# Performance work log

Hardware: AMD Instinct MI355X
Metric: run time of the kernel (lower is better)

The kernel has to match this reference:

```python
import jax, jax.numpy as jnp
import numpy as np

N_ING, N_DIR = 100000, 50000
E = 1000000
H, D = 4, 16          # heads, per-head dim
HID = H * D           # 64
LAT, COND = 32, 8
F_ING, F_DIR = 16, 8
OUT_ING = 16


def _han_edge(x_src, x_dst, att_s, att_d, edge_index, n_dst):
    # HANConv per-edge-type attention message passing.
    src, dst = edge_index[0], edge_index[1]
    a = jax.nn.leaky_relu(
        jnp.einsum('nhd,hd->nh', x_src, att_s)[src]
        + jnp.einsum('nhd,hd->nh', x_dst, att_d)[dst],
        negative_slope=0.2)                               # [E, H]
    amax = jax.ops.segment_max(a, dst, num_segments=n_dst)
    ex = jnp.exp(a - amax[dst])
    denom = jax.ops.segment_sum(ex, dst, num_segments=n_dst)
    alpha = ex / (denom[dst] + 1e-16)                     # PyG softmax eps
    out = jax.ops.segment_sum(x_src[src] * alpha[:, :, None], dst,
                              num_segments=n_dst)         # [n_dst, H, D]
    return jax.nn.relu(out.reshape(n_dst, HID))


def _group(outs, q, Wk, bk):
    # HANConv semantic-level attention across edge types.
    s = jnp.stack(outs)                                   # [T, N, HID]
    score = jnp.tanh(s @ Wk + bk).mean(axis=1) @ q        # [T]
    attn = jax.nn.softmax(score)
    return jnp.einsum('t,tnf->nf', attn, s)


def setup_inputs() -> dict:
    key = jax.random.key(0)
    ks = jax.random.split(key, 32)
    def ei(k, n_src, n_dst):
        k1, k2 = jax.random.split(k)
        return jnp.stack([jax.random.randint(k1, (E,), 0, n_src),
                          jax.random.randint(k2, (E,), 0, n_dst)]).astype(jnp.int64)
    s = 0.1
    inp = {
        'x_ing': jax.random.normal(ks[0], (N_ING, F_ING), jnp.float32),
        'x_dir': jax.random.normal(ks[1], (N_DIR, F_DIR), jnp.float32),
        'cond':  jax.random.normal(ks[2], (COND,), jnp.float32),
        'eps':   jax.random.normal(ks[3], (1, LAT), jnp.float32),
        'ei_cooc':     ei(ks[4], N_ING, N_DIR),
        'ei_used':     ei(ks[5], N_ING, N_DIR),
        'ei_contains': ei(ks[6], N_DIR, N_ING),
        'ei_pairs':    ei(ks[7], N_DIR, N_DIR),
        'ei_follows':  ei(ks[8], N_DIR, N_DIR),
        # node-type projections
        'W_pi': jax.random.normal(ks[9],  (F_ING, HID)) * s,
        'b_pi': jnp.zeros((HID,)),
        'W_pd': jax.random.normal(ks[10], (F_DIR, HID)) * s,
        'b_pd': jnp.zeros((HID,)),
        # semantic attention
        'Wk': jax.random.normal(ks[21], (HID, HID)) * s,
        'bk': jnp.zeros((HID,)),
        'q':  jax.random.normal(ks[22], (HID,)) * s,
        # VAE heads (input: 2*HID + COND)
        'W_mu': jax.random.normal(ks[23], (2 * HID + COND, LAT)) * s,
        'b_mu': jnp.zeros((LAT,)),
        'W_lv': jax.random.normal(ks[24], (2 * HID + COND, LAT)) * s,
        'b_lv': jnp.zeros((LAT,)),
        # decoder (fc1 is dead code in the original forward)
        'W_fc3': jax.random.normal(ks[25], (LAT, HID)) * s,
        'b_fc3': jnp.zeros((HID,)),
        'W_fc2': jax.random.normal(ks[26], (HID, OUT_ING)) * s,
        'b_fc2': jnp.zeros((OUT_ING,)),
    }
    for i, name in enumerate(['cooc', 'used', 'contains', 'pairs', 'follows']):
        inp[f'as_{name}'] = jax.random.normal(ks[11 + i], (H, D)) * s
        inp[f'ad_{name}'] = jax.random.normal(ks[16 + i], (H, D)) * s
    return inp


def reference(x_ing, x_dir, cond, eps,
              ei_cooc, ei_used, ei_contains, ei_pairs, ei_follows,
              W_pi, b_pi, W_pd, b_pd,
              as_cooc, ad_cooc, as_used, ad_used, as_contains, ad_contains,
              as_pairs, ad_pairs, as_follows, ad_follows,
              Wk, bk, q, W_mu, b_mu, W_lv, b_lv,
              W_fc3, b_fc3, W_fc2, b_fc2):
    # node-type projections -> [N, H, D]
    h_ing = (x_ing @ W_pi + b_pi).reshape(N_ING, H, D)
    h_dir = (x_dir @ W_pd + b_pd).reshape(N_DIR, H, D)

    o_cooc = _han_edge(h_ing, h_dir, as_cooc, ad_cooc, ei_cooc, N_DIR)
    o_used = _han_edge(h_ing, h_dir, as_used, ad_used, ei_used, N_DIR)
    o_cont = _han_edge(h_dir, h_ing, as_contains, ad_contains, ei_contains, N_ING)
    o_pair = _han_edge(h_dir, h_dir, as_pairs, ad_pairs, ei_pairs, N_DIR)
    o_foll = _han_edge(h_dir, h_dir, as_follows, ad_follows, ei_follows, N_DIR)

    out_ing = _group([o_cont], q, Wk, bk)                       # [N_ING, HID]
    out_dir = _group([o_cooc, o_used, o_pair, o_foll], q, Wk, bk)

    ingre_pool = out_ing.mean(axis=0, keepdims=True)            # [1, HID]
    direc_pool = out_dir.mean(axis=0, keepdims=True)
    graph_repr = jnp.concatenate([ingre_pool, direc_pool, cond[None]], axis=1)

    mu = graph_repr @ W_mu + b_mu
    logvar = graph_repr @ W_lv + b_lv
    z = mu + eps * jnp.exp(0.5 * logvar)

    # decoder: fc1 branch is overwritten in the original; effective path below
    recon = jnp.tanh(jax.nn.relu(z @ W_fc3 + b_fc3) @ W_fc2 + b_fc2)  # [1, OUT_ING]
    return recon, mu, logvar
```

## Files before the change

kernel.cpp:

```cpp
#include <hip/hip_runtime.h>
#include <hip/hip_fp16.h>
#include <math.h>

#define N_ING 100000
#define N_DIR 50000
#define NE    1000000
#define NDST_TOTAL 300000
#define NBUCK 4688
#define BA    16
#define NBK   (5 * BA)
#define I4PT  (NE / 4)
#define PB_ING 384
#define PB_DIR 192

typedef float v2f __attribute__((ext_vector_type(2)));

__global__ __launch_bounds__(256) void kA_kernel(
    const int* __restrict__ e0, const int* __restrict__ e1,
    const int* __restrict__ e2, const int* __restrict__ e3,
    const int* __restrict__ e4, int* __restrict__ blockcnt,
    const float* __restrict__ x_ing, const float* __restrict__ W_pi,
    const float* __restrict__ b_pi,
    const float* __restrict__ as_cooc, const float* __restrict__ as_used,
    const float* __restrict__ ad_contains,
    unsigned* __restrict__ h8_ing, __half* __restrict__ s_ing,
    const float* __restrict__ x_dir, const float* __restrict__ W_pd,
    const float* __restrict__ b_pd,
    const float* __restrict__ ad_cooc, const float* __restrict__ ad_used,
    const float* __restrict__ as_contains, const float* __restrict__ as_pairs,
    const float* __restrict__ ad_pairs, const float* __restrict__ as_follows,
    const float* __restrict__ ad_follows,
    unsigned* __restrict__ h8_dir, __half* __restrict__ s_dir)
{
    __shared__ int hist[NBUCK];
    __shared__ float sW[16 * 64];
    __shared__ float sbb[64];
    __shared__ float satt[7 * 64];
    __shared__ float sx[4][16];
    __shared__ float srow[4][64];

    const int bid = blockIdx.x;
    const int tid = threadIdx.x;
    if (bid < NBK) {
        const int type = bid / BA, blk = bid % BA;
        const int* ei = type == 0 ? e0 : type == 1 ? e1 : type == 2 ? e2
                      : type == 3 ? e3 : e4;
        const int base = type == 0 ? 0 : type == 1 ? 50000 : type == 2 ? 100000
                       : type == 3 ? 200000 : 250000;
        for (int i = tid; i < NBUCK; i += 256) hist[i] = 0;
        __syncthreads();
        const int4* d4 = (const int4*)(ei + NE);
        for (int i = blk * 256 + tid; i < I4PT; i += BA * 256) {
            int4 d = d4[i];
            atomicAdd(&hist[(base + d.x) >> 6], 1);
            atomicAdd(&hist[(base + d.y) >> 6], 1);
            atomicAdd(&hist[(base + d.z) >> 6], 1);
            atomicAdd(&hist[(base + d.w) >> 6], 1);
        }
        __syncthreads();
        int* row = blockcnt + (size_t)bid * NBUCK;
        for (int i = tid; i < NBUCK; i += 256) row[i] = hist[i];
    } else if (bid < NBK + PB_ING) {
        const int g = tid >> 6, t = tid & 63;
        for (int i = tid; i < 16 * 64; i += 256) sW[i] = W_pi[i];
        if (tid < 64) {
            sbb[tid] = b_pi[tid];
            satt[tid]       = as_cooc[tid];
            satt[64 + tid]  = as_used[tid];
            satt[128 + tid] = ad_contains[tid];
        }
        __syncthreads();
        for (int q = bid - NBK; q < N_ING / 4; q += PB_ING) {
            int n = q * 4 + g;
            if (t < 16) sx[g][t] = x_ing[(size_t)n * 16 + t];
            __syncthreads();
            float s = sbb[t];
#pragma unroll
            for (int i = 0; i < 16; ++i) s += sx[g][i] * sW[i * 64 + t];
            srow[g][t] = s;
            __syncthreads();
            if (t < 16) {
                int w0 = __builtin_amdgcn_cvt_pk_fp8_f32(srow[g][t * 4], srow[g][t * 4 + 1], 0, false);
                int w  = __builtin_amdgcn_cvt_pk_fp8_f32(srow[g][t * 4 + 2], srow[g][t * 4 + 3], w0, true);
                h8_ing[(size_t)n * 16 + t] = (unsigned)w;
            }
            if (t < 12) {
                int slot = t >> 2, hh = t & 3;
                float sc = 0.f;
#pragma unroll
                for (int d = 0; d < 16; ++d)
                    sc += srow[g][hh * 16 + d] * satt[slot * 64 + hh * 16 + d];
                s_ing[(size_t)n * 12 + t] = __float2half(sc);
            }
            __syncthreads();
        }
    } else {
        const int g = tid >> 6, t = tid & 63;
        for (int i = tid; i < 8 * 64; i += 256) sW[i] = W_pd[i];
        if (tid < 64) {
            sbb[tid] = b_pd[tid];
            satt[tid]        = ad_cooc[tid];
            satt[64  + tid]  = ad_used[tid];
            satt[128 + tid]  = as_contains[tid];
            satt[192 + tid]  = as_pairs[tid];
            satt[256 + tid]  = ad_pairs[tid];
            satt[320 + tid]  = as_follows[tid];
            satt[384 + tid]  = ad_follows[tid];
        }
        __syncthreads();
        for (int q = bid - NBK - PB_ING; q < N_DIR / 4; q += PB_DIR) {
            int n = q * 4 + g;
            if (t < 8) sx[g][t] = x_dir[(size_t)n * 8 + t];
            __syncthreads();
            float s = sbb[t];
#pragma unroll
            for (int i = 0; i < 8; ++i) s += sx[g][i] * sW[i * 64 + t];
            srow[g][t] = s;
            __syncthreads();
            if (t < 16) {
                int w0 = __builtin_amdgcn_cvt_pk_fp8_f32(srow[g][t * 4], srow[g][t * 4 + 1], 0, false);
                int w  = __builtin_amdgcn_cvt_pk_fp8_f32(srow[g][t * 4 + 2], srow[g][t * 4 + 3], w0, true);
                h8_dir[(size_t)n * 16 + t] = (unsigned)w;
            }
            if (t < 28) {
                int slot = t >> 2, hh = t & 3;
                float sc = 0.f;
#pragma unroll
                for (int d = 0; d < 16; ++d)
                    sc += srow[g][hh * 16 + d] * satt[slot * 64 + hh * 16 + d];
                s_dir[(size_t)n * 28 + t] = __float2half(sc);
            }
            __syncthreads();
        }
    }
}

__global__ __launch_bounds__(256) void k2_kernel(
    const int* __restrict__ blockcnt, int* __restrict__ blockbase,
    int* __restrict__ bbase, int* __restrict__ btot, int* __restrict__ cursor)
{
    __shared__ int part[4][64];
    __shared__ int tots[64];
    __shared__ int scn[64];
    __shared__ int bw;
    const int tid = threadIdx.x;
    const int kq = tid >> 6, bl = tid & 63;
    const int b = blockIdx.x * 64 + bl;
    const int K = NBK / 4;
    int ps = 0;
    if (b < NBUCK)
        for (int k = kq * K; k < kq * K + K; ++k)
            ps += blockcnt[(size_t)k * NBUCK + b];
    part[kq][bl] = ps;
    __syncthreads();
    if (tid < 64) {
        int t = part[0][tid] + part[1][tid] + part[2][tid] + part[3][tid];
        tots[tid] = t;
        scn[tid] = t;
    }
    __syncthreads();
    for (int off = 1; off < 64; off <<= 1) {
        int v = 0;
        if (tid < 64 && tid >= off) v = scn[tid - off];
        __syncthreads();
        if (tid < 64) scn[tid] += v;
        __syncthreads();
    }
    if (tid == 63) bw = atomicAdd(cursor, scn[63]);
    __syncthreads();
    if (b < NBUCK) {
        int bs = bw + scn[bl] - tots[bl];
        if (kq == 0) {
            bbase[b] = bs;
            btot[b] = tots[bl];
        }
        int run = bs;
        for (int q = 0; q < kq; ++q) run += part[q][bl];
        for (int k = kq * K; k < kq * K + K; ++k) {
            blockbase[(size_t)k * NBUCK + b] = run;
            run += blockcnt[(size_t)k * NBUCK + b];
        }
    }
}

__global__ __launch_bounds__(256) void k3_kernel(
    const int* __restrict__ e0, const int* __restrict__ e1,
    const int* __restrict__ e2, const int* __restrict__ e3,
    const int* __restrict__ e4, const int* __restrict__ blockbase,
    unsigned* __restrict__ bpair)
{
    __shared__ int cur[NBUCK];
    const int bid = blockIdx.x, tid = threadIdx.x;
    const int type = bid / BA, blk = bid % BA;
    const int* ei = type == 0 ? e0 : type == 1 ? e1 : type == 2 ? e2
                  : type == 3 ? e3 : e4;
    const int base = type == 0 ? 0 : type == 1 ? 50000 : type == 2 ? 100000
                   : type == 3 ? 200000 : 250000;
    const int* row = blockbase + (size_t)bid * NBUCK;
    for (int i = tid; i < NBUCK; i += 256) cur[i] = row[i];
    __syncthreads();
    const int4* s4 = (const int4*)ei;
    const int4* d4 = (const int4*)(ei + NE);
    for (int i = blk * 256 + tid; i < I4PT; i += BA * 256) {
        int4 s = s4[i];
        int4 d = d4[i];
        int g0 = base + d.x, g1 = base + d.y, g2 = base + d.z, g3 = base + d.w;
        int p0 = atomicAdd(&cur[g0 >> 6], 1);
        int p1 = atomicAdd(&cur[g1 >> 6], 1);
        int p2 = atomicAdd(&cur[g2 >> 6], 1);
        int p3 = atomicAdd(&cur[g3 >> 6], 1);
        bpair[p0] = ((unsigned)(g0 & 63) << 17) | (unsigned)s.x;
        bpair[p1] = ((unsigned)(g1 & 63) << 17) | (unsigned)s.y;
        bpair[p2] = ((unsigned)(g2 & 63) << 17) | (unsigned)s.z;
        bpair[p3] = ((unsigned)(g3 & 63) << 17) | (unsigned)s.w;
    }
}

__global__ __launch_bounds__(256) void k4_kernel(
    const unsigned* __restrict__ bpair, const int* __restrict__ bbase,
    const int* __restrict__ btot, int* __restrict__ perm,
    int* __restrict__ start, int* __restrict__ cnt)
{
    __shared__ int h[64], sc[64], cu[64];
    const int b = blockIdx.x, tid = threadIdx.x;
    const int jb = bbase[b], n = btot[b];
    if (tid < 64) h[tid] = 0;
    __syncthreads();
    for (int i = tid; i < n; i += 256)
        atomicAdd(&h[bpair[jb + i] >> 17], 1);
    __syncthreads();
    if (tid == 0) {
        int r = 0;
        for (int i = 0; i < 64; ++i) { sc[i] = r; cu[i] = r; r += h[i]; }
    }
    __syncthreads();
    if (tid < 64) {
        int dg = b * 64 + tid;
        if (dg < NDST_TOTAL) {
            start[dg] = jb + sc[tid];
            cnt[dg] = h[tid];
        }
    }
    for (int i = tid; i < n; i += 256) {
        unsigned p = bpair[jb + i];
        int pos = atomicAdd(&cu[p >> 17], 1);
        perm[jb + pos] = (int)(p & 0x1FFFF);
    }
}

__global__ __launch_bounds__(256) void agg_all_kernel(
    const int* __restrict__ perm, const int* __restrict__ start,
    const int* __restrict__ cnttot,
    const unsigned* __restrict__ h8_ing, const unsigned* __restrict__ h8_dir,
    const __half* __restrict__ s_ing, const __half* __restrict__ s_dir,
    const float* __restrict__ Wk, const float* __restrict__ bk,
    float* __restrict__ pool_ing, float* __restrict__ pool_dir,
    float* __restrict__ sem_dir)
{
    __shared__ float sWk[64 * 64];
    __shared__ float srow[4][64];
    __shared__ float sred[4][64];
    const int t = threadIdx.x & 63, w = threadIdx.x >> 6;
    const int g  = t >> 4;
    const int l4 = t & 15;
    const int hq = l4 >> 2;
    for (int i = threadIdx.x; i < 4096; i += 256) sWk[i] = Wk[i];
    const float bkf = bk[t];
    float p_ing = 0.f;
    float p0 = 0.f, p1 = 0.f, p2 = 0.f, p3 = 0.f;
    float m0 = 0.f, m1 = 0.f, m2 = 0.f, m3 = 0.f;
    __syncthreads();
    const int nwaves = gridDim.x * 4;
    for (int d = blockIdx.x * 4 + w; d < NDST_TOTAL; d += nwaves) {
        int type, ld;
        const __half *ssrc, *sdst;
        const unsigned* hsrc;
        int ss, soff, ds, doff;
        if (d < 50000)       { type = 0; ld = d;          ssrc = s_ing; ss = 12; soff = 0;  sdst = s_dir; ds = 28; doff = 0;  hsrc = h8_ing; }
        else if (d < 100000) { type = 1; ld = d - 50000;  ssrc = s_ing; ss = 12; soff = 4;  sdst = s_dir; ds = 28; doff = 4;  hsrc = h8_ing; }
        else if (d < 200000) { type = 2; ld = d - 100000; ssrc = s_dir; ss = 28; soff = 8;  sdst = s_ing; ds = 12; doff = 8;  hsrc = h8_dir; }
        else if (d < 250000) { type = 3; ld = d - 200000; ssrc = s_dir; ss = 28; soff = 12; sdst = s_dir; ds = 28; doff = 16; hsrc = h8_dir; }
        else                 { type = 4; ld = d - 250000; ssrc = s_dir; ss = 28; soff = 20; sdst = s_dir; ds = 28; doff = 24; hsrc = h8_dir; }
        float adst = __half2float(sdst[(size_t)ld * ds + doff + hq]);
        int jb = start[d], je = jb + cnttot[d];
        float4 acc = make_float4(0.f, 0.f, 0.f, 0.f);
        float dsum = 0.f;
        for (int j = jb; j < je; j += 8) {
            int j0 = j + g, j1 = j + 4 + g;
            bool v0 = j0 < je, v1 = j1 < je;
            int s0 = perm[v0 ? j0 : je - 1];
            int s1 = perm[v1 ? j1 : je - 1];
            float c0 = __half2float(ssrc[(size_t)s0 * ss + soff + hq]);
            float c1 = __half2float(ssrc[(size_t)s1 * ss + soff + hq]);
            unsigned u0 = hsrc[(size_t)s0 * 16 + l4];
            unsigned u1 = hsrc[(size_t)s1 * 16 + l4];
            float a0 = c0 + adst; a0 = a0 > 0.f ? a0 : 0.2f * a0;
            float a1 = c1 + adst; a1 = a1 > 0.f ? a1 : 0.2f * a1;
            float e0 = v0 ? __expf(a0) : 0.f;
            float e1 = v1 ? __expf(a1) : 0.f;
            dsum += e0 + e1;
            v2f lo0 = __builtin_amdgcn_cvt_pk_f32_fp8((int)u0, false);
            v2f hi0 = __builtin_amdgcn_cvt_pk_f32_fp8((int)u0, true);
            v2f lo1 = __builtin_amdgcn_cvt_pk_f32_fp8((int)u1, false);
            v2f hi1 = __builtin_amdgcn_cvt_pk_f32_fp8((int)u1, true);
            acc.x += lo0.x * e0 + lo1.x * e1;
            acc.y += lo0.y * e0 + lo1.y * e1;
            acc.z += hi0.x * e0 + hi1.x * e1;
            acc.w += hi0.y * e0 + hi1.y * e1;
        }
#pragma unroll
        for (int mask = 16; mask <= 32; mask <<= 1) {
            acc.x += __shfl_xor(acc.x, mask, 64);
            acc.y += __shfl_xor(acc.y, mask, 64);
            acc.z += __shfl_xor(acc.z, mask, 64);
            acc.w += __shfl_xor(acc.w, mask, 64);
            dsum  += __shfl_xor(dsum,  mask, 64);
        }
        float inv = 1.f / (dsum + 1e-16f);
        float4 v4 = make_float4(fmaxf(acc.x * inv, 0.f), fmaxf(acc.y * inv, 0.f),
                                fmaxf(acc.z * inv, 0.f), fmaxf(acc.w * inv, 0.f));
        if (g == 0) *(float4*)&srow[w][l4 * 4] = v4;
        float v = srow[w][t];
        if (type == 2) {
            p_ing += v;
        } else {
            float a2 = bkf;
#pragma unroll
            for (int k = 0; k < 64; ++k) a2 += srow[w][k] * sWk[k * 64 + t];
            float tv = tanhf(a2);
            if (type == 0)      { p0 += v; m0 += tv; }
            else if (type == 1) { p1 += v; m1 += tv; }
            else if (type == 3) { p2 += v; m2 += tv; }
            else                { p3 += v; m3 += tv; }
        }
    }
    float vals[9] = { p_ing, p0, p1, p2, p3, m0, m1, m2, m3 };
    float* outs[9] = { pool_ing, pool_dir, pool_dir + 64, pool_dir + 128,
                       pool_dir + 192, sem_dir, sem_dir + 64, sem_dir + 128,
                       sem_dir + 192 };
    for (int i = 0; i < 9; ++i) {
        __syncthreads();
        sred[w][t] = vals[i];
        __syncthreads();
        if (w == 0)
            atomicAdd(&outs[i][t], sred[0][t] + sred[1][t] + sred[2][t] + sred[3][t]);
    }
}

__global__ __launch_bounds__(64) void final_kernel(
    const float* __restrict__ pool_ing, const float* __restrict__ pool_dir,
    const float* __restrict__ sem_dir, const float* __restrict__ q,
    const float* __restrict__ cond, const float* __restrict__ eps,
    const float* __restrict__ W_mu, const float* __restrict__ b_mu,
    const float* __restrict__ W_lv, const float* __restrict__ b_lv,
    const float* __restrict__ W_fc3, const float* __restrict__ b_fc3,
    const float* __restrict__ W_fc2, const float* __restrict__ b_fc2,
    float* __restrict__ out)
{
    __shared__ float gr[136];
    __shared__ float sc[4], attn[4];
    __shared__ float z[32], hfc[64];
    int t = threadIdx.x;
    if (t < 4) {
        float s = 0.f;
        for (int f = 0; f < 64; ++f)
            s += (sem_dir[t * 64 + f] / (float)N_DIR) * q[f];
        sc[t] = s;
    }
    gr[t] = pool_ing[t] / (float)N_ING;
    __syncthreads();
    if (t == 0) {
        float m = fmaxf(fmaxf(sc[0], sc[1]), fmaxf(sc[2], sc[3]));
        float ssum = 0.f;
        for (int i = 0; i < 4; ++i) { attn[i] = expf(sc[i] - m); ssum += attn[i]; }
        for (int i = 0; i < 4; ++i) attn[i] /= ssum;
    }
    __syncthreads();
    {
        float v = 0.f;
        for (int tt = 0; tt < 4; ++tt)
            v += attn[tt] * (pool_dir[tt * 64 + t] / (float)N_DIR);
        gr[64 + t] = v;
    }
    if (t < 8) gr[128 + t] = cond[t];
    __syncthreads();
    if (t < 32) {
        float m = b_mu[t], lv = b_lv[t];
        for (int i = 0; i < 136; ++i) {
            float g = gr[i];
            m  += g * W_mu[i * 32 + t];
            lv += g * W_lv[i * 32 + t];
        }
        out[16 + t] = m;
        out[48 + t] = lv;
        z[t] = m + eps[t] * expf(0.5f * lv);
    }
    __syncthreads();
    {
        float v = b_fc3[t];
        for (int j = 0; j < 32; ++j) v += z[j] * W_fc3[j * 64 + t];
        hfc[t] = fmaxf(v, 0.f);
    }
    __syncthreads();
    if (t < 16) {
        float v = b_fc2[t];
        for (int f = 0; f < 64; ++f) v += hfc[f] * W_fc2[f * 16 + t];
        out[t] = tanhf(v);
    }
}

extern "C" void kernel_launch(void* const* d_in, const int* in_sizes, int n_in,
                              void* d_out, int out_size, void* d_ws, size_t ws_size,
                              hipStream_t stream) {
    const float* x_ing = (const float*)d_in[0];
    const float* x_dir = (const float*)d_in[1];
    const float* cond  = (const float*)d_in[2];
    const float* eps   = (const float*)d_in[3];
    const int* ei_cooc     = (const int*)d_in[4];
    const int* ei_used     = (const int*)d_in[5];
    const int* ei_contains = (const int*)d_in[6];
    const int* ei_pairs    = (const int*)d_in[7];
    const int* ei_follows  = (const int*)d_in[8];
    const float* W_pi = (const float*)d_in[9];
    const float* b_pi = (const float*)d_in[10];
    const float* W_pd = (const float*)d_in[11];
    const float* b_pd = (const float*)d_in[12];
    const float* Wk   = (const float*)d_in[13];
    const float* bk   = (const float*)d_in[14];
    const float* q    = (const float*)d_in[15];
    const float* W_mu = (const float*)d_in[16];
    const float* b_mu = (const float*)d_in[17];
    const float* W_lv = (const float*)d_in[18];
    const float* b_lv = (const float*)d_in[19];
    const float* W_fc3 = (const float*)d_in[20];
    const float* b_fc3 = (const float*)d_in[21];
    const float* W_fc2 = (const float*)d_in[22];
    const float* b_fc2 = (const float*)d_in[23];
    const float* as_cooc     = (const float*)d_in[24];
    const float* ad_cooc     = (const float*)d_in[25];
    const float* as_used     = (const float*)d_in[26];
    const float* ad_used     = (const float*)d_in[27];
    const float* as_contains = (const float*)d_in[28];
    const float* ad_contains = (const float*)d_in[29];
    const float* as_pairs    = (const float*)d_in[30];
    const float* ad_pairs    = (const float*)d_in[31];
    const float* as_follows  = (const float*)d_in[32];
    const float* ad_follows  = (const float*)d_in[33];

    unsigned* bpair = (unsigned*)d_ws;
    unsigned* h8_ing = bpair + (size_t)5 * NE;
    unsigned* h8_dir = h8_ing + (size_t)N_ING * 16;
    __half* s_ing = (__half*)(h8_dir + (size_t)N_DIR * 16);
    __half* s_dir = s_ing + (size_t)N_ING * 12;
    int*   perm  = (int*)(s_dir + (size_t)N_DIR * 28);
    int*   blockcnt  = perm + (size_t)5 * NE;
    int*   blockbase = blockcnt + (size_t)NBK * NBUCK;
    int*   bbase  = blockbase + (size_t)NBK * NBUCK;
    int*   btot   = bbase + NBUCK;
    int*   start  = btot + NBUCK;
    int*   cnt    = start + NDST_TOTAL;
    int*   cursor = cnt + NDST_TOTAL;
    float* pool_ing = (float*)(cursor + 1);
    float* pool_dir = pool_ing + 64;
    float* sem_dir  = pool_dir + 256;

    hipMemsetAsync(cursor, 0, (1 + 64 + 256 + 256) * sizeof(int), stream);

    kA_kernel<<<NBK + PB_ING + PB_DIR, 256, 0, stream>>>(
        ei_cooc, ei_used, ei_contains, ei_pairs, ei_follows, blockcnt,
        x_ing, W_pi, b_pi, as_cooc, as_used, ad_contains, h8_ing, s_ing,
        x_dir, W_pd, b_pd, ad_cooc, ad_used, as_contains, as_pairs, ad_pairs,
        as_follows, ad_follows, h8_dir, s_dir);

    k2_kernel<<<(NBUCK + 63) / 64, 256, 0, stream>>>(
        blockcnt, blockbase, bbase, btot, cursor);

    k3_kernel<<<NBK, 256, 0, stream>>>(
        ei_cooc, ei_used, ei_contains, ei_pairs, ei_follows, blockbase, bpair);

    k4_kernel<<<NBUCK, 256, 0, stream>>>(bpair, bbase, btot, perm, start, cnt);

    agg_all_kernel<<<2048, 256, 0, stream>>>(
        perm, start, cnt, h8_ing, h8_dir, s_ing, s_dir, Wk, bk,
        pool_ing, pool_dir, sem_dir);

    final_kernel<<<1, 64, 0, stream>>>(
        pool_ing, pool_dir, sem_dir, q, cond, eps,
        W_mu, b_mu, W_lv, b_lv, W_fc3, b_fc3, W_fc2, b_fc2, (float*)d_out);
}
```

Baseline: 541.2 us.

## Keep Wk column in registers, use exp2 with prescaled scores, 32-bit indexing

```diff
diff --git a/kernel.cpp b/kernel.cpp
--- a/kernel.cpp
+++ b/kernel.cpp
@@ -12,6 +12,7 @@
 #define I4PT  (NE / 4)
 #define PB_ING 384
 #define PB_DIR 192
+#define LOG2E 1.442695041f
 
 typedef float v2f __attribute__((ext_vector_type(2)));
 
@@ -65,9 +66,9 @@
         for (int i = tid; i < 16 * 64; i += 256) sW[i] = W_pi[i];
         if (tid < 64) {
             sbb[tid] = b_pi[tid];
-            satt[tid]       = as_cooc[tid];
-            satt[64 + tid]  = as_used[tid];
-            satt[128 + tid] = ad_contains[tid];
+            satt[tid]       = as_cooc[tid] * LOG2E;
+            satt[64 + tid]  = as_used[tid] * LOG2E;
+            satt[128 + tid] = ad_contains[tid] * LOG2E;
         }
         __syncthreads();
         for (int q = bid - NBK; q < N_ING / 4; q += PB_ING) {
@@ -99,13 +100,13 @@
         for (int i = tid; i < 8 * 64; i += 256) sW[i] = W_pd[i];
         if (tid < 64) {
             sbb[tid] = b_pd[tid];
-            satt[tid]        = ad_cooc[tid];
-            satt[64  + tid]  = ad_used[tid];
-            satt[128 + tid]  = as_contains[tid];
-            satt[192 + tid]  = as_pairs[tid];
-            satt[256 + tid]  = ad_pairs[tid];
-            satt[320 + tid]  = as_follows[tid];
-            satt[384 + tid]  = ad_follows[tid];
+            satt[tid]        = ad_cooc[tid] * LOG2E;
+            satt[64  + tid]  = ad_used[tid] * LOG2E;
+            satt[128 + tid]  = as_contains[tid] * LOG2E;
+            satt[192 + tid]  = as_pairs[tid] * LOG2E;
+            satt[256 + tid]  = ad_pairs[tid] * LOG2E;
+            satt[320 + tid]  = as_follows[tid] * LOG2E;
+            satt[384 + tid]  = ad_follows[tid] * LOG2E;
         }
         __syncthreads();
         for (int q = bid - NBK - PB_ING; q < N_DIR / 4; q += PB_DIR) {
@@ -248,7 +249,7 @@
     }
 }
 
-__global__ __launch_bounds__(256) void agg_all_kernel(
+__global__ __launch_bounds__(256, 4) void agg_all_kernel(
     const int* __restrict__ perm, const int* __restrict__ start,
     const int* __restrict__ cnttot,
     const unsigned* __restrict__ h8_ing, const unsigned* __restrict__ h8_dir,
@@ -257,47 +258,50 @@
     float* __restrict__ pool_ing, float* __restrict__ pool_dir,
     float* __restrict__ sem_dir)
 {
-    __shared__ float sWk[64 * 64];
-    __shared__ float srow[4][64];
+    __shared__ __align__(16) float srow[4][64];
     __shared__ float sred[4][64];
     const int t = threadIdx.x & 63, w = threadIdx.x >> 6;
     const int g  = t >> 4;
     const int l4 = t & 15;
     const int hq = l4 >> 2;
-    for (int i = threadIdx.x; i < 4096; i += 256) sWk[i] = Wk[i];
+
+    float wkc[64];
+#pragma unroll
+    for (int k = 0; k < 64; ++k) wkc[k] = Wk[k * 64 + t];
     const float bkf = bk[t];
+
     float p_ing = 0.f;
     float p0 = 0.f, p1 = 0.f, p2 = 0.f, p3 = 0.f;
     float m0 = 0.f, m1 = 0.f, m2 = 0.f, m3 = 0.f;
-    __syncthreads();
     const int nwaves = gridDim.x * 4;
     for (int d = blockIdx.x * 4 + w; d < NDST_TOTAL; d += nwaves) {
         int type, ld;
         const __half *ssrc, *sdst;
         const unsigned* hsrc;
-        int ss, soff, ds, doff;
-        if (d < 50000)       { type = 0; ld = d;          ssrc = s_ing; ss = 12; soff = 0;  sdst = s_dir; ds = 28; doff = 0;  hsrc = h8_ing; }
-        else if (d < 100000) { type = 1; ld = d - 50000;  ssrc = s_ing; ss = 12; soff = 4;  sdst = s_dir; ds = 28; doff = 4;  hsrc = h8_ing; }
-        else if (d < 200000) { type = 2; ld = d - 100000; ssrc = s_dir; ss = 28; soff = 8;  sdst = s_ing; ds = 12; doff = 8;  hsrc = h8_dir; }
-        else if (d < 250000) { type = 3; ld = d - 200000; ssrc = s_dir; ss = 28; soff = 12; sdst = s_dir; ds = 28; doff = 16; hsrc = h8_dir; }
-        else                 { type = 4; ld = d - 250000; ssrc = s_dir; ss = 28; soff = 20; sdst = s_dir; ds = 28; doff = 24; hsrc = h8_dir; }
-        float adst = __half2float(sdst[(size_t)ld * ds + doff + hq]);
+        unsigned uss, uds; int soff, doff;
+        if (d < 50000)       { type = 0; ld = d;          ssrc = s_ing; uss = 12; soff = 0;  sdst = s_dir; uds = 28; doff = 0;  hsrc = h8_ing; }
+        else if (d < 100000) { type = 1; ld = d - 50000;  ssrc = s_ing; uss = 12; soff = 4;  sdst = s_dir; uds = 28; doff = 4;  hsrc = h8_ing; }
+        else if (d < 200000) { type = 2; ld = d - 100000; ssrc = s_dir; uss = 28; soff = 8;  sdst = s_ing; uds = 12; doff = 8;  hsrc = h8_dir; }
+        else if (d < 250000) { type = 3; ld = d - 200000; ssrc = s_dir; uss = 28; soff = 12; sdst = s_dir; uds = 28; doff = 16; hsrc = h8_dir; }
+        else                 { type = 4; ld = d - 250000; ssrc = s_dir; uss = 28; soff = 20; sdst = s_dir; uds = 28; doff = 24; hsrc = h8_dir; }
+        float adst = __half2float(sdst[(unsigned)ld * uds + (unsigned)(doff + hq)]);
+        const unsigned usoff = (unsigned)(soff + hq);
         int jb = start[d], je = jb + cnttot[d];
         float4 acc = make_float4(0.f, 0.f, 0.f, 0.f);
         float dsum = 0.f;
         for (int j = jb; j < je; j += 8) {
             int j0 = j + g, j1 = j + 4 + g;
             bool v0 = j0 < je, v1 = j1 < je;
-            int s0 = perm[v0 ? j0 : je - 1];
-            int s1 = perm[v1 ? j1 : je - 1];
-            float c0 = __half2float(ssrc[(size_t)s0 * ss + soff + hq]);
-            float c1 = __half2float(ssrc[(size_t)s1 * ss + soff + hq]);
-            unsigned u0 = hsrc[(size_t)s0 * 16 + l4];
-            unsigned u1 = hsrc[(size_t)s1 * 16 + l4];
+            unsigned s0 = (unsigned)perm[v0 ? j0 : je - 1];
+            unsigned s1 = (unsigned)perm[v1 ? j1 : je - 1];
+            float c0 = __half2float(ssrc[s0 * uss + usoff]);
+            float c1 = __half2float(ssrc[s1 * uss + usoff]);
+            unsigned u0 = hsrc[s0 * 16u + (unsigned)l4];
+            unsigned u1 = hsrc[s1 * 16u + (unsigned)l4];
             float a0 = c0 + adst; a0 = a0 > 0.f ? a0 : 0.2f * a0;
             float a1 = c1 + adst; a1 = a1 > 0.f ? a1 : 0.2f * a1;
-            float e0 = v0 ? __expf(a0) : 0.f;
-            float e1 = v1 ? __expf(a1) : 0.f;
+            float e0 = v0 ? __builtin_amdgcn_exp2f(a0) : 0.f;
+            float e1 = v1 ? __builtin_amdgcn_exp2f(a1) : 0.f;
             dsum += e0 + e1;
             v2f lo0 = __builtin_amdgcn_cvt_pk_f32_fp8((int)u0, false);
             v2f hi0 = __builtin_amdgcn_cvt_pk_f32_fp8((int)u0, true);
@@ -326,7 +330,11 @@
         } else {
             float a2 = bkf;
 #pragma unroll
-            for (int k = 0; k < 64; ++k) a2 += srow[w][k] * sWk[k * 64 + t];
+            for (int kq = 0; kq < 16; ++kq) {
+                float4 sr = *(const float4*)&srow[w][kq * 4];
+                a2 += sr.x * wkc[4 * kq]     + sr.y * wkc[4 * kq + 1]
+                    + sr.z * wkc[4 * kq + 2] + sr.w * wkc[4 * kq + 3];
+            }
             float tv = tanhf(a2);
             if (type == 0)      { p0 += v; m0 += tv; }
             else if (type == 1) { p1 += v; m1 += tv; }
```

New measurement: 597.1 us. +10.3%, slower.
